# Kernel tuning notes

Measured on AMD Instinct MI355X. Metric: run time of the kernel, lower is better.

Reference implementation:

```python
import jax, jax.numpy as jnp
import numpy as np

B = 131072          # points on manifold
A = 16              # n_anchors
SDIM = 512          # substrate.n (spatial dim); ambient dim = SDIM + 1
ALPHA = 0.1         # attraction coefficient
EPS = 1e-7


def _proj(p):
    # Project onto hyperboloid: recompute time coord from spatial part.
    sp = p[..., 1:]
    t = jnp.sqrt(1.0 + jnp.sum(sp * sp, axis=-1, keepdims=True))
    return jnp.concatenate([t, sp], axis=-1)


def _linner(x, y):
    # Lorentz inner product <x,y>_L = -x0*y0 + sum_i xi*yi
    return -x[..., 0] * y[..., 0] + jnp.sum(x[..., 1:] * y[..., 1:], axis=-1)


def setup_inputs() -> dict:
    key = jax.random.key(0)
    k1, k2 = jax.random.split(key)
    x_sp = jax.random.normal(k1, (B, SDIM), dtype=jnp.float32)
    x = _proj(jnp.concatenate([jnp.zeros((B, 1), jnp.float32), x_sp], axis=-1))
    a_sp = jax.random.normal(k2, (A, SDIM), dtype=jnp.float32) * 0.01
    anchors = _proj(jnp.concatenate([jnp.zeros((A, 1), jnp.float32), a_sp], axis=-1))
    return {"x": x, "anchors": anchors}


def reference(x, anchors):
    af = _proj(anchors)                                   # [A, D]
    D = af.shape[-1]
    metric = jnp.concatenate([-jnp.ones((1,), x.dtype), jnp.ones((D - 1,), x.dtype)])
    # pairwise -<x,a>_L  -> [B, A]
    theta_all = -jnp.einsum('bd,ad->ba', x * metric, af)
    dists = jnp.arccosh(jnp.clip(theta_all, 1.0 + EPS, None))
    idx = jnp.argmin(dists, axis=1)                       # nearest anchor per point
    y = af[idx]                                           # [B, D]
    # log_map_x(y) = acosh(theta)/sqrt(theta^2-1) * (y - theta*x)
    theta = jnp.clip(-_linner(x, y), 1.0 + EPS, None)[:, None]
    direction = (jnp.arccosh(theta) / jnp.sqrt(theta * theta - 1.0)) * (y - theta * x)
    v = ALPHA * direction                                 # tangent vector
    # exp_map_x(v) = cosh(||v||_L) x + sinh(||v||_L)/||v||_L * v
    vn = jnp.sqrt(jnp.clip(_linner(v, v), EPS, None))[:, None]
    return jnp.cosh(vn) * x + (jnp.sinh(vn) / vn) * v
```

## Files before the change

### kernel.cpp

```cpp
#include <hip/hip_runtime.h>

#define NA 16
#define DD 513
#define ALPHA 0.1f
#define EPSV 1e-7f
#define TPW 2
#define GRID 1024

typedef __fp16 h2v __attribute__((ext_vector_type(2)));
typedef __fp16 f16x8 __attribute__((ext_vector_type(8)));
typedef float f32x4 __attribute__((ext_vector_type(4)));
typedef unsigned int u32;

union H2U { h2v h; u32 u; };
union FU  { float f; u32 u; int i; };
union FRAG { u32 w[4]; f16x8 v; };
union U4   { uint4 v; u32 w[4]; };

static __device__ __forceinline__ u32 pkrtz(float lo, float hi) {
    H2U t; t.h = __builtin_amdgcn_cvt_pkrtz(lo, hi); return t.u;
}
static __device__ __forceinline__ h2v asH2(u32 w) { H2U t; t.u = w; return t.h; }

static __device__ __forceinline__ int swz(int G) {
    return G ^ (((G >> 4) & 3) | (((G >> 6) & 1) << 2));
}

__global__ __launch_bounds__(256, 2)
void hfield_kernel(const float* __restrict__ x,
                   const float* __restrict__ anc,
                   float* __restrict__ out) {
    __shared__ uint4 bframe[1024];
    __shared__ uint4 xframe[4][1024];

    const int tid = threadIdx.x, lane = tid & 63, wid = tid >> 6;
    const int col = lane & 15, g = lane >> 4;

    const int rowbase0 = (blockIdx.x * 4 + wid) * (16 * TPW);
    const float* xb = x + (size_t)rowbase0 * DD;
    uint4* xf = xframe[wid];

    float nv[16][8];
#pragma unroll
    for (int r = 0; r < 16; ++r) {
        const float* p = xb + (size_t)r * DD + 1 + lane;
#pragma unroll
        for (int j = 0; j < 8; ++j) nv[r][j] = p[64 * j];
    }
    float x0r[TPW][4];
#pragma unroll
    for (int t = 0; t < TPW; ++t)
#pragma unroll
        for (int r4 = 0; r4 < 4; ++r4)
            x0r[t][r4] = xb[(size_t)(t * 16 + 4 * g + r4) * DD];
    __builtin_amdgcn_sched_barrier(0);

#pragma unroll
    for (int m = 0; m < 4; ++m) {
        const int F = m * 256 + tid;
        const int l = F & 63, kt = F >> 6;
        const int a = l & 15, lp = 4 * kt + (l >> 4);
        const float* p = anc + a * DD + 1 + lp;
        uint4 w;
        w.x = pkrtz(p[0],   p[64]);
        w.y = pkrtz(p[128], p[192]);
        w.z = pkrtz(p[256], p[320]);
        w.w = pkrtz(p[384], p[448]);
        bframe[swz(F)] = w;
    }

    float af0c;
    {
        const float* p = anc + col * DD + 1 + g * 128;
        float s = 0.f;
#pragma unroll 16
        for (int i = 0; i < 128; ++i) s = fmaf(p[i], p[i], s);
        s += __shfl_xor(s, 16);
        s += __shfl_xor(s, 32);
        af0c = sqrtf(1.0f + s);
    }
    __syncthreads();

    const float thmin = 1.0f + 1e-7f;

#pragma unroll
    for (int t = 0; t < TPW; ++t) {
        const int rowbase = rowbase0 + t * 16;

        if (t > 0)
            asm volatile("s_waitcnt lgkmcnt(0)" ::: "memory");
#pragma unroll
        for (int r = 0; r < 16; ++r) {
            uint4 w;
            w.x = pkrtz(nv[r][0], nv[r][1]);
            w.y = pkrtz(nv[r][2], nv[r][3]);
            w.z = pkrtz(nv[r][4], nv[r][5]);
            w.w = pkrtz(nv[r][6], nv[r][7]);
            xf[swz((lane >> 2) * 64 + 16 * (lane & 3) + r)] = w;
        }

        if (t + 1 < TPW) {
            const float* nb = xb + (size_t)((t + 1) * 16) * DD;
#pragma unroll
            for (int r = 0; r < 16; ++r) {
                const float* p = nb + (size_t)r * DD + 1 + lane;
#pragma unroll
                for (int j = 0; j < 8; ++j) nv[r][j] = p[64 * j];
            }
            __builtin_amdgcn_sched_barrier(0);
        }

        asm volatile("s_waitcnt lgkmcnt(0)" ::: "memory");

        f32x4 acc = {0.f, 0.f, 0.f, 0.f};
#pragma unroll
        for (int kt = 0; kt < 16; ++kt) {
            FRAG A, B;
            U4 ax, bx;
            ax.v = xf[swz(kt * 64 + lane)];
            bx.v = bframe[swz(kt * 64 + lane)];
            A.w[0] = ax.w[0]; A.w[1] = ax.w[1]; A.w[2] = ax.w[2]; A.w[3] = ax.w[3];
            B.w[0] = bx.w[0]; B.w[1] = bx.w[1]; B.w[2] = bx.w[2]; B.w[3] = bx.w[3];
            acc = __builtin_amdgcn_mfma_f32_16x16x32_f16(A.v, B.v, acc, 0, 0, 0);
        }

        float c1r[4], c2r[4], o0r[4];
        int bir[4];
#pragma unroll
        for (int r4 = 0; r4 < 4; ++r4) {
            const float th = fmaxf(fmaf(x0r[t][r4], af0c, -acc[r4]), thmin);
            FU u; u.f = th;
            u32 key = (u.u & 0xFFFFFFF0u) | (u32)col;
#pragma unroll
            for (int m = 1; m <= 8; m <<= 1) {
                const u32 o = (u32)__shfl_xor((int)key, m);
                key = o < key ? o : key;
            }
            const int bi  = (int)(key & 15u);
            const int src = (lane & 48) | bi;
            const float thw = __shfl(th, src);
            const float y0  = __shfl(af0c, src);

            const float s2 = thw * thw - 1.0f;
            const float rr = sqrtf(s2);
            const float ac = __logf(thw + rr);
            const float cf = ac / rr;
            const float vn = sqrtf(fmaxf(ALPHA * ALPHA * ac * ac, EPSV));
            const float e  = __expf(vn);
            const float ei = 1.0f / e;
            const float ch = 0.5f * (e + ei);
            const float sh = 0.5f * (e - ei);
            const float c2 = ALPHA * cf * (sh / vn);
            const float c1 = fmaf(-c2, thw, ch);

            c1r[r4] = c1;
            c2r[r4] = c2;
            o0r[r4] = fmaf(c2, y0, c1 * x0r[t][r4]);
            bir[r4] = bi;
        }

#pragma unroll 4
        for (int r = 0; r < 16; ++r) {
            const int src = (r >> 2) * 16;
            const float c1 = __shfl(c1r[r & 3], src);
            const float c2 = __shfl(c2r[r & 3], src);
            const float o0 = __shfl(o0r[r & 3], src);
            const int   bi = __builtin_amdgcn_readfirstlane(__shfl(bir[r & 3], src));

            U4 X, Y;
            X.v = xf[swz((lane >> 2) * 64 + 16 * (lane & 3) + r)];
            Y.v = bframe[swz((lane >> 2) * 64 + 16 * (lane & 3) + bi)];

            float* op = out + (size_t)(rowbase + r) * DD;
            if (lane == 0) __builtin_nontemporal_store(o0, op);
#pragma unroll
            for (int q = 0; q < 4; ++q) {
                const h2v hx = asH2(X.w[q]);
                const h2v hy = asH2(Y.w[q]);
                __builtin_nontemporal_store(fmaf(c2, (float)hy.x, c1 * (float)hx.x),
                                            &op[1 + lane + 128 * q]);
                __builtin_nontemporal_store(fmaf(c2, (float)hy.y, c1 * (float)hx.y),
                                            &op[1 + lane + 64 + 128 * q]);
            }
        }
    }
}

extern "C" void kernel_launch(void* const* d_in, const int* in_sizes, int n_in,
                              void* d_out, int out_size, void* d_ws, size_t ws_size,
                              hipStream_t stream) {
    const float* x   = (const float*)d_in[0];
    const float* anc = (const float*)d_in[1];
    float* out       = (float*)d_out;
    hipLaunchKernelGGL(hfield_kernel, dim3(GRID), dim3(256), 0, stream, x, anc, out);
}
```

Measured before the change: 111.1 us.

## Switch to 8-row tiles with 16-byte vector loads and stores and a new LDS layout

```diff
diff --git a/kernel.cpp b/kernel.cpp
--- a/kernel.cpp
+++ b/kernel.cpp
@@ -4,12 +4,13 @@
 #define DD 513
 #define ALPHA 0.1f
 #define EPSV 1e-7f
-#define TPW 2
+#define TPW 4
 #define GRID 1024
 
 typedef __fp16 h2v __attribute__((ext_vector_type(2)));
 typedef __fp16 f16x8 __attribute__((ext_vector_type(8)));
 typedef float f32x4 __attribute__((ext_vector_type(4)));
+typedef float f32x4u __attribute__((ext_vector_type(4), aligned(4)));
 typedef unsigned int u32;
 
 union H2U { h2v h; u32 u; };
@@ -22,51 +23,44 @@
 }
 static __device__ __forceinline__ h2v asH2(u32 w) { H2U t; t.u = w; return t.h; }
 
-static __device__ __forceinline__ int swz(int G) {
-    return G ^ (((G >> 4) & 3) | (((G >> 6) & 1) << 2));
-}
-
-__global__ __launch_bounds__(256, 2)
+struct __attribute__((packed, aligned(4))) F4 { float x, y, z, w; };
+
+
+__global__ __launch_bounds__(256, 3)
 void hfield_kernel(const float* __restrict__ x,
                    const float* __restrict__ anc,
                    float* __restrict__ out) {
-    __shared__ uint4 bframe[1024];
-    __shared__ uint4 xframe[4][1024];
+    __shared__ uint4 bframe[NA * 64];
+    __shared__ uint4 xframe[4][8 * 64];
 
     const int tid = threadIdx.x, lane = tid & 63, wid = tid >> 6;
     const int col = lane & 15, g = lane >> 4;
 
-    const int rowbase0 = (blockIdx.x * 4 + wid) * (16 * TPW);
+    const int rowbase0 = (blockIdx.x * 4 + wid) * (8 * TPW);
     const float* xb = x + (size_t)rowbase0 * DD;
     uint4* xf = xframe[wid];
 
-    float nv[16][8];
-#pragma unroll
-    for (int r = 0; r < 16; ++r) {
-        const float* p = xb + (size_t)r * DD + 1 + lane;
-#pragma unroll
-        for (int j = 0; j < 8; ++j) nv[r][j] = p[64 * j];
-    }
-    float x0r[TPW][4];
-#pragma unroll
-    for (int t = 0; t < TPW; ++t)
-#pragma unroll
-        for (int r4 = 0; r4 < 4; ++r4)
-            x0r[t][r4] = xb[(size_t)(t * 16 + 4 * g + r4) * DD];
+    F4 nvA[8], nvB[8];
+#pragma unroll
+    for (int r = 0; r < 8; ++r) {
+        const float* p = xb + (size_t)r * DD + 1 + 4 * lane;
+        nvA[r] = *(const F4*)p;
+        nvB[r] = *(const F4*)(p + 256);
+    }
     __builtin_amdgcn_sched_barrier(0);
 
 #pragma unroll
     for (int m = 0; m < 4; ++m) {
-        const int F = m * 256 + tid;
-        const int l = F & 63, kt = F >> 6;
-        const int a = l & 15, lp = 4 * kt + (l >> 4);
-        const float* p = anc + a * DD + 1 + lp;
+        const int i = m * 256 + tid;
+        const int a = i >> 6, u = i & 63;
+        const float* p = anc + a * DD + 1 + 4 * u;
+        const float* q = p + 256;
         uint4 w;
-        w.x = pkrtz(p[0],   p[64]);
-        w.y = pkrtz(p[128], p[192]);
-        w.z = pkrtz(p[256], p[320]);
-        w.w = pkrtz(p[384], p[448]);
-        bframe[swz(F)] = w;
+        w.x = pkrtz(p[0], p[1]);
+        w.y = pkrtz(p[2], p[3]);
+        w.z = pkrtz(q[0], q[1]);
+        w.w = pkrtz(q[2], q[3]);
+        bframe[a * 64 + (u ^ (a & 7))] = w;
     }
 
     float af0c;
@@ -83,42 +77,44 @@
 
     const float thmin = 1.0f + 1e-7f;
 
-#pragma unroll
+#pragma unroll 1
     for (int t = 0; t < TPW; ++t) {
-        const int rowbase = rowbase0 + t * 16;
-
-        if (t > 0)
-            asm volatile("s_waitcnt lgkmcnt(0)" ::: "memory");
-#pragma unroll
-        for (int r = 0; r < 16; ++r) {
+        const int rowbase = rowbase0 + t * 8;
+
+#pragma unroll
+        for (int r = 0; r < 8; ++r) {
             uint4 w;
-            w.x = pkrtz(nv[r][0], nv[r][1]);
-            w.y = pkrtz(nv[r][2], nv[r][3]);
-            w.z = pkrtz(nv[r][4], nv[r][5]);
-            w.w = pkrtz(nv[r][6], nv[r][7]);
-            xf[swz((lane >> 2) * 64 + 16 * (lane & 3) + r)] = w;
+            w.x = pkrtz(nvA[r].x, nvA[r].y);
+            w.y = pkrtz(nvA[r].z, nvA[r].w);
+            w.z = pkrtz(nvB[r].x, nvB[r].y);
+            w.w = pkrtz(nvB[r].z, nvB[r].w);
+            xf[r * 64 + (lane ^ (r & 7))] = w;
         }
 
         if (t + 1 < TPW) {
-            const float* nb = xb + (size_t)((t + 1) * 16) * DD;
-#pragma unroll
-            for (int r = 0; r < 16; ++r) {
-                const float* p = nb + (size_t)r * DD + 1 + lane;
-#pragma unroll
-                for (int j = 0; j < 8; ++j) nv[r][j] = p[64 * j];
+            const float* nb = xb + (size_t)((t + 1) * 8) * DD;
+#pragma unroll
+            for (int r = 0; r < 8; ++r) {
+                const float* p = nb + (size_t)r * DD + 1 + 4 * lane;
+                nvA[r] = *(const F4*)p;
+                nvB[r] = *(const F4*)(p + 256);
             }
             __builtin_amdgcn_sched_barrier(0);
         }
 
-        asm volatile("s_waitcnt lgkmcnt(0)" ::: "memory");
+        float x0r[4];
+#pragma unroll
+        for (int r4 = 0; r4 < 4; ++r4)
+            x0r[r4] = xb[(size_t)(t * 8 + ((4 * g + r4) & 7)) * DD];
 
         f32x4 acc = {0.f, 0.f, 0.f, 0.f};
 #pragma unroll
         for (int kt = 0; kt < 16; ++kt) {
+            const int u = 4 * kt + g;
             FRAG A, B;
             U4 ax, bx;
-            ax.v = xf[swz(kt * 64 + lane)];
-            bx.v = bframe[swz(kt * 64 + lane)];
+            ax.v = xf[(col & 7) * 64 + (u ^ (col & 7))];
+            bx.v = bframe[col * 64 + (u ^ (col & 7))];
             A.w[0] = ax.w[0]; A.w[1] = ax.w[1]; A.w[2] = ax.w[2]; A.w[3] = ax.w[3];
             B.w[0] = bx.w[0]; B.w[1] = bx.w[1]; B.w[2] = bx.w[2]; B.w[3] = bx.w[3];
             acc = __builtin_amdgcn_mfma_f32_16x16x32_f16(A.v, B.v, acc, 0, 0, 0);
@@ -128,7 +124,7 @@
         int bir[4];
 #pragma unroll
         for (int r4 = 0; r4 < 4; ++r4) {
-            const float th = fmaxf(fmaf(x0r[t][r4], af0c, -acc[r4]), thmin);
+            const float th = fmaxf(fmaf(x0r[r4], af0c, -acc[r4]), thmin);
             FU u; u.f = th;
             u32 key = (u.u & 0xFFFFFFF0u) | (u32)col;
 #pragma unroll
@@ -155,12 +151,12 @@
 
             c1r[r4] = c1;
             c2r[r4] = c2;
-            o0r[r4] = fmaf(c2, y0, c1 * x0r[t][r4]);
+            o0r[r4] = fmaf(c2, y0, c1 * x0r[r4]);
             bir[r4] = bi;
         }
 
-#pragma unroll 4
-        for (int r = 0; r < 16; ++r) {
+#pragma unroll
+        for (int r = 0; r < 8; ++r) {
             const int src = (r >> 2) * 16;
             const float c1 = __shfl(c1r[r & 3], src);
             const float c2 = __shfl(c2r[r & 3], src);
@@ -168,20 +164,28 @@
             const int   bi = __builtin_amdgcn_readfirstlane(__shfl(bir[r & 3], src));
 
             U4 X, Y;
-            X.v = xf[swz((lane >> 2) * 64 + 16 * (lane & 3) + r)];
-            Y.v = bframe[swz((lane >> 2) * 64 + 16 * (lane & 3) + bi)];
-
-            float* op = out + (size_t)(rowbase + r) * DD;
-            if (lane == 0) __builtin_nontemporal_store(o0, op);
-#pragma unroll
-            for (int q = 0; q < 4; ++q) {
+            X.v = xf[r * 64 + (lane ^ (r & 7))];
+            Y.v = bframe[bi * 64 + (lane ^ (bi & 7))];
+
+            f32x4u s0, s1;
+#pragma unroll
+            for (int q = 0; q < 2; ++q) {
                 const h2v hx = asH2(X.w[q]);
                 const h2v hy = asH2(Y.w[q]);
-                __builtin_nontemporal_store(fmaf(c2, (float)hy.x, c1 * (float)hx.x),
-                                            &op[1 + lane + 128 * q]);
-                __builtin_nontemporal_store(fmaf(c2, (float)hy.y, c1 * (float)hx.y),
-                                            &op[1 + lane + 64 + 128 * q]);
-            }
+                s0[2 * q]     = fmaf(c2, (float)hy.x, c1 * (float)hx.x);
+                s0[2 * q + 1] = fmaf(c2, (float)hy.y, c1 * (float)hx.y);
+            }
+#pragma unroll
+            for (int q = 0; q < 2; ++q) {
+                const h2v hx = asH2(X.w[2 + q]);
+                const h2v hy = asH2(Y.w[2 + q]);
+                s1[2 * q]     = fmaf(c2, (float)hy.x, c1 * (float)hx.x);
+                s1[2 * q + 1] = fmaf(c2, (float)hy.y, c1 * (float)hx.y);
+            }
+            float* op = out + (size_t)(rowbase + r) * DD;
+            __builtin_nontemporal_store(s0, (f32x4u*)(op + 1 + 4 * lane));
+            __builtin_nontemporal_store(s1, (f32x4u*)(op + 257 + 4 * lane));
+            if (lane == 0) __builtin_nontemporal_store(o0, op);
         }
     }
 }
```

After: 103.9 us. 1.07x faster.
